# Performance work log

Hardware: AMD Instinct MI355X
Metric: run time of the kernel (lower is better)

The kernel has to match this reference:

```python
import jax, jax.numpy as jnp
import numpy as np

N = 8192      # nodes
F = 256       # in_features
H = 64        # hidden_dim
NEG = -9e15   # mask fill value from the torch source
EPS = 1e-5    # LayerNorm eps (torch default)


def setup_inputs() -> dict:
    key = jax.random.key(0)
    ks = jax.random.split(key, 6)
    x = jax.random.normal(ks[0], (N, F), jnp.float32)
    adj = jax.random.randint(ks[1], (N, N), 0, 2, jnp.int32)
    # Linear params (xavier-ish scale, zero bias as in reset_parameters)
    Wt = jax.random.normal(ks[2], (H, F), jnp.float32) * (1.0 / np.sqrt(F))
    bt = jnp.zeros((H,), jnp.float32)
    Wa = jax.random.normal(ks[3], (1, H), jnp.float32) * (1.0 / np.sqrt(H))
    ba = jnp.zeros((1,), jnp.float32)
    Wp = jax.random.normal(ks[4], (F, H), jnp.float32) * (1.0 / np.sqrt(H))
    bp = jnp.zeros((F,), jnp.float32)
    gamma = jnp.ones((F,), jnp.float32)
    beta = jnp.zeros((F,), jnp.float32)
    return dict(x=x, adj=adj, Wt=Wt, bt=bt, Wa=Wa, ba=ba,
                Wp=Wp, bp=bp, gamma=gamma, beta=beta)


def reference(x, adj, Wt, bt, Wa, ba, Wp, bp, gamma, beta):
    # h = feature_transform(x): [N, H]
    h = x @ Wt.T + bt
    # per-source-node scalar score, expanded over all N columns: [N, 1]
    s = jax.nn.leaky_relu(h @ Wa.T + ba, negative_slope=0.2)
    # adjacency-masked softmax over neighbors (dim=1); s broadcasts to [N, N]
    scores = jnp.where(adj > 0, s, jnp.float32(NEG))
    w = jax.nn.softmax(scores, axis=1)            # [N, N]
    # dropout inactive at inference -> identity
    neighbor = w @ h                               # [N, H]
    tf = neighbor @ Wp.T + bp                      # [N, F]
    # residual + LayerNorm
    y = x + tf
    mu = jnp.mean(y, axis=-1, keepdims=True)
    var = jnp.var(y, axis=-1, keepdims=True)
    return gamma * (y - mu) * jax.lax.rsqrt(var + EPS) + beta
```

## Files before the change

### kernel.cpp

```cpp
#include <hip/hip_runtime.h>
#include <stdint.h>

#define NN 8192
#define FF 256
#define HH 64

typedef __attribute__((ext_vector_type(8))) short bf16x8;
typedef __attribute__((ext_vector_type(4))) float f32x4;

__device__ __forceinline__ uint16_t f2bf(float f) {
  union { float f; uint32_t i; } c; c.f = f;
  uint32_t r = c.i + 0x7FFFu + ((c.i >> 16) & 1u);
  return (uint16_t)(r >> 16);
}

__global__ __launch_bounds__(256) void k1_h(
    const float* __restrict__ x, const float* __restrict__ Wt,
    const float* __restrict__ bt, uint16_t* __restrict__ hT) {
  __shared__ float wtT[256 * 65];
  __shared__ float sbt[64];
  __shared__ uint16_t s_tr[64][34];
  const int t = threadIdx.x;
  const int lane = t & 63;
  const int w = t >> 6;

  for (int i = 0; i < 64; ++i)
    wtT[t * 65 + i] = Wt[(size_t)i * FF + t];
  if (t < 64) sbt[t] = bt[t];
  __syncthreads();

  const int n0 = blockIdx.x * 32;
  const int r0 = n0 + w * 8;
  const float binit = sbt[lane];
  float acc[8];
#pragma unroll
  for (int r = 0; r < 8; ++r) acc[r] = binit;

  for (int f4 = 0; f4 < FF; f4 += 4) {
    float4 xs[8];
#pragma unroll
    for (int r = 0; r < 8; ++r)
      xs[r] = *(const float4*)(x + (size_t)(r0 + r) * FF + f4);
    const float wt0 = wtT[(f4 + 0) * 65 + lane];
    const float wt1 = wtT[(f4 + 1) * 65 + lane];
    const float wt2 = wtT[(f4 + 2) * 65 + lane];
    const float wt3 = wtT[(f4 + 3) * 65 + lane];
#pragma unroll
    for (int r = 0; r < 8; ++r)
      acc[r] += xs[r].x * wt0 + xs[r].y * wt1 + xs[r].z * wt2 + xs[r].w * wt3;
  }

#pragma unroll
  for (int r = 0; r < 8; ++r)
    s_tr[lane][w * 8 + r] = f2bf(acc[r]);
  __syncthreads();
#pragma unroll
  for (int i = 0; i < 4; ++i) {
    int idx = i * 256 + t;
    int c = idx >> 4;
    int d = idx & 15;
    uint32_t v = (uint32_t)s_tr[c][2 * d] | ((uint32_t)s_tr[c][2 * d + 1] << 16);
    *(uint32_t*)(hT + (size_t)c * NN + n0 + 2 * d) = v;
  }
}

__global__ __launch_bounds__(256) void k2_attn(
    const int* __restrict__ adj, const uint16_t* __restrict__ hT,
    float* __restrict__ nb_part, int* __restrict__ deg_part) {
  __shared__ float s_part[4][16][64];
  __shared__ int   s_deg[16];

  const int t    = threadIdx.x;
  const int w    = t >> 6;
  const int lane = t & 63;
  const int m    = lane & 15;
  const int q    = lane >> 4;
  const int g    = blockIdx.x >> 1;
  const int half = blockIdx.x & 1;
  const int row0 = g * 16;

  if (t < 16) s_deg[t] = 0;
  __syncthreads();

  const int kbeg = half * (NN / 2) + w * (NN / 8);
  const int kend = kbeg + (NN / 8);

  f32x4 acc0 = 0, acc1 = 0, acc2 = 0, acc3 = 0;
  uint32_t degp = 0;
  const int* __restrict__ arow = adj + (size_t)(row0 + m) * NN;
  const uint16_t* __restrict__ hrow = hT + (size_t)m * NN;

  for (int kb = kbeg; kb < kend; kb += 64) {
    const int k0 = kb + q * 8;
    const int k1 = k0 + 32;
    int4 a0 = *(const int4*)(arow + k0);
    int4 a1 = *(const int4*)(arow + k0 + 4);
    int4 a2 = *(const int4*)(arow + k1);
    int4 a3 = *(const int4*)(arow + k1 + 4);
    bf16x8 b0 = *(const bf16x8*)(hrow + k0);
    bf16x8 b1 = *(const bf16x8*)(hrow + 16 * NN + k0);
    bf16x8 b2 = *(const bf16x8*)(hrow + 32 * NN + k0);
    bf16x8 b3 = *(const bf16x8*)(hrow + 48 * NN + k0);
    bf16x8 c0 = *(const bf16x8*)(hrow + k1);
    bf16x8 c1 = *(const bf16x8*)(hrow + 16 * NN + k1);
    bf16x8 c2 = *(const bf16x8*)(hrow + 32 * NN + k1);
    bf16x8 c3 = *(const bf16x8*)(hrow + 48 * NN + k1);
    uint32_t p0 = (uint32_t)a0.x | ((uint32_t)a0.y << 16);
    uint32_t p1 = (uint32_t)a0.z | ((uint32_t)a0.w << 16);
    uint32_t p2 = (uint32_t)a1.x | ((uint32_t)a1.y << 16);
    uint32_t p3 = (uint32_t)a1.z | ((uint32_t)a1.w << 16);
    uint32_t p4 = (uint32_t)a2.x | ((uint32_t)a2.y << 16);
    uint32_t p5 = (uint32_t)a2.z | ((uint32_t)a2.w << 16);
    uint32_t p6 = (uint32_t)a3.x | ((uint32_t)a3.y << 16);
    uint32_t p7 = (uint32_t)a3.z | ((uint32_t)a3.w << 16);
    union U { bf16x8 v; uint32_t u[4]; } afA, afB;
    afA.u[0] = p0 * 0x3F80u;
    afA.u[1] = p1 * 0x3F80u;
    afA.u[2] = p2 * 0x3F80u;
    afA.u[3] = p3 * 0x3F80u;
    afB.u[0] = p4 * 0x3F80u;
    afB.u[1] = p5 * 0x3F80u;
    afB.u[2] = p6 * 0x3F80u;
    afB.u[3] = p7 * 0x3F80u;
    degp += p0 + p1 + p2 + p3 + p4 + p5 + p6 + p7;
    acc0 = __builtin_amdgcn_mfma_f32_16x16x32_bf16(afA.v, b0, acc0, 0, 0, 0);
    acc1 = __builtin_amdgcn_mfma_f32_16x16x32_bf16(afA.v, b1, acc1, 0, 0, 0);
    acc2 = __builtin_amdgcn_mfma_f32_16x16x32_bf16(afA.v, b2, acc2, 0, 0, 0);
    acc3 = __builtin_amdgcn_mfma_f32_16x16x32_bf16(afA.v, b3, acc3, 0, 0, 0);
    acc0 = __builtin_amdgcn_mfma_f32_16x16x32_bf16(afB.v, c0, acc0, 0, 0, 0);
    acc1 = __builtin_amdgcn_mfma_f32_16x16x32_bf16(afB.v, c1, acc1, 0, 0, 0);
    acc2 = __builtin_amdgcn_mfma_f32_16x16x32_bf16(afB.v, c2, acc2, 0, 0, 0);
    acc3 = __builtin_amdgcn_mfma_f32_16x16x32_bf16(afB.v, c3, acc3, 0, 0, 0);
  }

  int degm = (int)(degp & 0xFFFFu) + (int)(degp >> 16);
  degm += __shfl_down(degm, 32, 64);
  degm += __shfl_down(degm, 16, 64);
  if (lane < 16) atomicAdd(&s_deg[lane], degm);

#pragma unroll
  for (int rg = 0; rg < 4; ++rg) {
    s_part[w][q * 4 + rg][ 0 + m] = acc0[rg];
    s_part[w][q * 4 + rg][16 + m] = acc1[rg];
    s_part[w][q * 4 + rg][32 + m] = acc2[rg];
    s_part[w][q * 4 + rg][48 + m] = acc3[rg];
  }
  __syncthreads();

  float* __restrict__ dst = nb_part + ((size_t)half * NN + row0) * HH;
  for (int idx = t; idx < 16 * 64; idx += 256) {
    int r = idx >> 6, c = idx & 63;
    float s = s_part[0][r][c] + s_part[1][r][c] +
              s_part[2][r][c] + s_part[3][r][c];
    dst[(size_t)r * HH + c] = s;
  }
  if (t < 16) deg_part[half * NN + row0 + t] = s_deg[t];
}

__global__ __launch_bounds__(256) void k3_epi(
    const float* __restrict__ x, const float* __restrict__ nb_part,
    const int* __restrict__ deg_part, const float* __restrict__ Wp,
    const float* __restrict__ bp, const float* __restrict__ gamma,
    const float* __restrict__ beta, float* __restrict__ out) {
  __shared__ float s_nb[16][64];
  __shared__ float s_y[16 * 256];

  const int t    = threadIdx.x;
  const int w    = t >> 6;
  const int lane = t & 63;
  const int row0 = blockIdx.x * 16;

  for (int idx = t; idx < 16 * 64; idx += 256) {
    int r = idx >> 6, c = idx & 63;
    int d = deg_part[row0 + r] + deg_part[NN + row0 + r];
    float s = nb_part[(size_t)(row0 + r) * HH + c] +
              nb_part[(size_t)(NN + row0 + r) * HH + c];
    s_nb[r][c] = (d > 0) ? s / (float)d : 0.f;
  }
  __syncthreads();

  {
    const int f = t;
    float wp[64];
    const float* wrow = Wp + (size_t)f * HH;
#pragma unroll
    for (int j = 0; j < 16; ++j) {
      float4 v = *(const float4*)(wrow + j * 4);
      wp[j * 4 + 0] = v.x; wp[j * 4 + 1] = v.y;
      wp[j * 4 + 2] = v.z; wp[j * 4 + 3] = v.w;
    }
    const float bpf = bp[f];
    for (int r = 0; r < 16; ++r) {
      float a = bpf;
#pragma unroll
      for (int k = 0; k < 64; k += 4) {
        float4 nv = *(const float4*)&s_nb[r][k];
        a += nv.x * wp[k] + nv.y * wp[k + 1] + nv.z * wp[k + 2] + nv.w * wp[k + 3];
      }
      float y = x[(size_t)(row0 + r) * FF + f] + a;
      s_y[r * 256 + f] = y;
    }
  }
  __syncthreads();

  for (int i = 0; i < 4; ++i) {
    const int r = w * 4 + i;
    float4 v = *(const float4*)&s_y[r * 256 + lane * 4];
    float sum = v.x + v.y + v.z + v.w;
    float ss  = v.x * v.x + v.y * v.y + v.z * v.z + v.w * v.w;
#pragma unroll
    for (int o = 32; o >= 1; o >>= 1) {
      sum += __shfl_xor(sum, o, 64);
      ss  += __shfl_xor(ss, o, 64);
    }
    const float mu  = sum * (1.0f / 256.0f);
    const float var = ss * (1.0f / 256.0f) - mu * mu;
    const float rs  = rsqrtf(var + 1e-5f);
    const int f0 = lane * 4;
    float4 g = *(const float4*)(gamma + f0);
    float4 b = *(const float4*)(beta + f0);
    float4 o4;
    o4.x = g.x * (v.x - mu) * rs + b.x;
    o4.y = g.y * (v.y - mu) * rs + b.y;
    o4.z = g.z * (v.z - mu) * rs + b.z;
    o4.w = g.w * (v.w - mu) * rs + b.w;
    *(float4*)(out + (size_t)(row0 + r) * FF + f0) = o4;
  }
}

extern "C" void kernel_launch(void* const* d_in, const int* in_sizes, int n_in,
                              void* d_out, int out_size, void* d_ws, size_t ws_size,
                              hipStream_t stream) {
  const float* x     = (const float*)d_in[0];
  const int*   adj   = (const int*)d_in[1];
  const float* Wt    = (const float*)d_in[2];
  const float* bt    = (const float*)d_in[3];
  const float* Wp    = (const float*)d_in[6];
  const float* bp    = (const float*)d_in[7];
  const float* gamma = (const float*)d_in[8];
  const float* beta  = (const float*)d_in[9];
  float* out = (float*)d_out;

  uint16_t* hT       = (uint16_t*)d_ws;
  float*    nb_part  = (float*)((char*)d_ws + (1u << 20));
  int*      deg_part = (int*)((char*)d_ws + (5u << 20));

  k1_h  <<<256,  256, 0, stream>>>(x, Wt, bt, hT);
  k2_attn<<<1024, 256, 0, stream>>>(adj, hT, nb_part, deg_part);
  k3_epi <<<512,  256, 0, stream>>>(x, nb_part, deg_part, Wp, bp, gamma, beta, out);
}
```

Baseline: 450.4 us.

## Fuse attention aggregation with epilogue and stage adjacency through swizzled LDS

```diff
diff --git a/kernel.cpp b/kernel.cpp
--- a/kernel.cpp
+++ b/kernel.cpp
@@ -64,80 +64,80 @@
   }
 }
 
-__global__ __launch_bounds__(256) void k2_attn(
+__global__ __launch_bounds__(256) void k2f(
     const int* __restrict__ adj, const uint16_t* __restrict__ hT,
-    float* __restrict__ nb_part, int* __restrict__ deg_part) {
-  __shared__ float s_part[4][16][64];
-  __shared__ int   s_deg[16];
+    const float* __restrict__ x, const float* __restrict__ Wp,
+    const float* __restrict__ bp, const float* __restrict__ gamma,
+    const float* __restrict__ beta, float* __restrict__ out) {
+  __shared__ __align__(16) unsigned char smem[49408];
+  unsigned char* af = smem;
+  float (*s_part)[16][64] = (float (*)[16][64])(smem + 32768);
+  float (*s_degw)[16]     = (float (*)[16])(smem + 32768 + 16384);
+  float (*s_nb)[64]       = (float (*)[64])(smem);
+  float* s_y              = (float*)(smem + 4096);
 
   const int t    = threadIdx.x;
   const int w    = t >> 6;
   const int lane = t & 63;
   const int m    = lane & 15;
   const int q    = lane >> 4;
-  const int g    = blockIdx.x >> 1;
-  const int half = blockIdx.x & 1;
-  const int row0 = g * 16;
-
-  if (t < 16) s_deg[t] = 0;
-  __syncthreads();
-
-  const int kbeg = half * (NN / 2) + w * (NN / 8);
-  const int kend = kbeg + (NN / 8);
-
-  f32x4 acc0 = 0, acc1 = 0, acc2 = 0, acc3 = 0;
-  uint32_t degp = 0;
-  const int* __restrict__ arow = adj + (size_t)(row0 + m) * NN;
+  const int row0 = blockIdx.x * 16;
+
+  bf16x8 vone;
+#pragma unroll
+  for (int j = 0; j < 8; ++j) vone[j] = (short)0x3F80;
+
+  f32x4 acc0 = 0, acc1 = 0, acc2 = 0, acc3 = 0, accd = 0;
   const uint16_t* __restrict__ hrow = hT + (size_t)m * NN;
-
-  for (int kb = kbeg; kb < kend; kb += 64) {
-    const int k0 = kb + q * 8;
-    const int k1 = k0 + 32;
-    int4 a0 = *(const int4*)(arow + k0);
-    int4 a1 = *(const int4*)(arow + k0 + 4);
-    int4 a2 = *(const int4*)(arow + k1);
-    int4 a3 = *(const int4*)(arow + k1 + 4);
-    bf16x8 b0 = *(const bf16x8*)(hrow + k0);
-    bf16x8 b1 = *(const bf16x8*)(hrow + 16 * NN + k0);
-    bf16x8 b2 = *(const bf16x8*)(hrow + 32 * NN + k0);
-    bf16x8 b3 = *(const bf16x8*)(hrow + 48 * NN + k0);
-    bf16x8 c0 = *(const bf16x8*)(hrow + k1);
-    bf16x8 c1 = *(const bf16x8*)(hrow + 16 * NN + k1);
-    bf16x8 c2 = *(const bf16x8*)(hrow + 32 * NN + k1);
-    bf16x8 c3 = *(const bf16x8*)(hrow + 48 * NN + k1);
-    uint32_t p0 = (uint32_t)a0.x | ((uint32_t)a0.y << 16);
-    uint32_t p1 = (uint32_t)a0.z | ((uint32_t)a0.w << 16);
-    uint32_t p2 = (uint32_t)a1.x | ((uint32_t)a1.y << 16);
-    uint32_t p3 = (uint32_t)a1.z | ((uint32_t)a1.w << 16);
-    uint32_t p4 = (uint32_t)a2.x | ((uint32_t)a2.y << 16);
-    uint32_t p5 = (uint32_t)a2.z | ((uint32_t)a2.w << 16);
-    uint32_t p6 = (uint32_t)a3.x | ((uint32_t)a3.y << 16);
-    uint32_t p7 = (uint32_t)a3.z | ((uint32_t)a3.w << 16);
-    union U { bf16x8 v; uint32_t u[4]; } afA, afB;
-    afA.u[0] = p0 * 0x3F80u;
-    afA.u[1] = p1 * 0x3F80u;
-    afA.u[2] = p2 * 0x3F80u;
-    afA.u[3] = p3 * 0x3F80u;
-    afB.u[0] = p4 * 0x3F80u;
-    afB.u[1] = p5 * 0x3F80u;
-    afB.u[2] = p6 * 0x3F80u;
-    afB.u[3] = p7 * 0x3F80u;
-    degp += p0 + p1 + p2 + p3 + p4 + p5 + p6 + p7;
-    acc0 = __builtin_amdgcn_mfma_f32_16x16x32_bf16(afA.v, b0, acc0, 0, 0, 0);
-    acc1 = __builtin_amdgcn_mfma_f32_16x16x32_bf16(afA.v, b1, acc1, 0, 0, 0);
-    acc2 = __builtin_amdgcn_mfma_f32_16x16x32_bf16(afA.v, b2, acc2, 0, 0, 0);
-    acc3 = __builtin_amdgcn_mfma_f32_16x16x32_bf16(afA.v, b3, acc3, 0, 0, 0);
-    acc0 = __builtin_amdgcn_mfma_f32_16x16x32_bf16(afB.v, c0, acc0, 0, 0, 0);
-    acc1 = __builtin_amdgcn_mfma_f32_16x16x32_bf16(afB.v, c1, acc1, 0, 0, 0);
-    acc2 = __builtin_amdgcn_mfma_f32_16x16x32_bf16(afB.v, c2, acc2, 0, 0, 0);
-    acc3 = __builtin_amdgcn_mfma_f32_16x16x32_bf16(afB.v, c3, acc3, 0, 0, 0);
-  }
-
-  int degm = (int)(degp & 0xFFFFu) + (int)(degp >> 16);
-  degm += __shfl_down(degm, 32, 64);
-  degm += __shfl_down(degm, 16, 64);
-  if (lane < 16) atomicAdd(&s_deg[lane], degm);
-
+  const int rsw = (m & 7) << 4;
+
+  for (int tile = 0; tile < 8; ++tile) {
+    const int c0 = tile * 1024;
+#pragma unroll
+    for (int i = 0; i < 16; ++i) {
+      int4 a = *(const int4*)(adj + (size_t)(row0 + i) * NN + c0 + t * 4);
+      uint32_t lo = ((uint32_t)a.x | ((uint32_t)a.y << 16)) * 0x3F80u;
+      uint32_t hi = ((uint32_t)a.z | ((uint32_t)a.w << 16)) * 0x3F80u;
+      uint2 w2; w2.x = lo; w2.y = hi;
+      uint32_t boff = (uint32_t)(t * 8) ^ (uint32_t)((i & 7) << 4);
+      *(uint2*)(af + (i << 11) + boff) = w2;
+    }
+    __syncthreads();
+#pragma unroll
+    for (int it = 0; it < 4; ++it) {
+      const int kl = w * 256 + it * 64;
+      const int k0 = c0 + kl + q * 8;
+      const int k1 = k0 + 32;
+      bf16x8 afA = *(const bf16x8*)(af + (m << 11) +
+                                    ((uint32_t)((kl + q * 8) * 2) ^ rsw));
+      bf16x8 afB = *(const bf16x8*)(af + (m << 11) +
+                                    ((uint32_t)((kl + q * 8 + 32) * 2) ^ rsw));
+      bf16x8 b0 = *(const bf16x8*)(hrow + k0);
+      bf16x8 b1 = *(const bf16x8*)(hrow + 16 * NN + k0);
+      bf16x8 b2 = *(const bf16x8*)(hrow + 32 * NN + k0);
+      bf16x8 b3 = *(const bf16x8*)(hrow + 48 * NN + k0);
+      bf16x8 d0 = *(const bf16x8*)(hrow + k1);
+      bf16x8 d1 = *(const bf16x8*)(hrow + 16 * NN + k1);
+      bf16x8 d2 = *(const bf16x8*)(hrow + 32 * NN + k1);
+      bf16x8 d3 = *(const bf16x8*)(hrow + 48 * NN + k1);
+      acc0 = __builtin_amdgcn_mfma_f32_16x16x32_bf16(afA, b0, acc0, 0, 0, 0);
+      acc1 = __builtin_amdgcn_mfma_f32_16x16x32_bf16(afA, b1, acc1, 0, 0, 0);
+      acc2 = __builtin_amdgcn_mfma_f32_16x16x32_bf16(afA, b2, acc2, 0, 0, 0);
+      acc3 = __builtin_amdgcn_mfma_f32_16x16x32_bf16(afA, b3, acc3, 0, 0, 0);
+      accd = __builtin_amdgcn_mfma_f32_16x16x32_bf16(afA, vone, accd, 0, 0, 0);
+      acc0 = __builtin_amdgcn_mfma_f32_16x16x32_bf16(afB, d0, acc0, 0, 0, 0);
+      acc1 = __builtin_amdgcn_mfma_f32_16x16x32_bf16(afB, d1, acc1, 0, 0, 0);
+      acc2 = __builtin_amdgcn_mfma_f32_16x16x32_bf16(afB, d2, acc2, 0, 0, 0);
+      acc3 = __builtin_amdgcn_mfma_f32_16x16x32_bf16(afB, d3, acc3, 0, 0, 0);
+      accd = __builtin_amdgcn_mfma_f32_16x16x32_bf16(afB, vone, accd, 0, 0, 0);
+    }
+    __syncthreads();
+  }
+
+#pragma unroll
+  for (int rg = 0; rg < 4; ++rg) {
+    (*s_part)[0][0] = (*s_part)[0][0];
+  }
 #pragma unroll
   for (int rg = 0; rg < 4; ++rg) {
     s_part[w][q * 4 + rg][ 0 + m] = acc0[rg];
@@ -145,37 +145,18 @@
     s_part[w][q * 4 + rg][32 + m] = acc2[rg];
     s_part[w][q * 4 + rg][48 + m] = acc3[rg];
   }
-  __syncthreads();
-
-  float* __restrict__ dst = nb_part + ((size_t)half * NN + row0) * HH;
+  if (m == 0) {
+#pragma unroll
+    for (int rg = 0; rg < 4; ++rg) s_degw[w][q * 4 + rg] = accd[rg];
+  }
+  __syncthreads();
+
   for (int idx = t; idx < 16 * 64; idx += 256) {
     int r = idx >> 6, c = idx & 63;
     float s = s_part[0][r][c] + s_part[1][r][c] +
               s_part[2][r][c] + s_part[3][r][c];
-    dst[(size_t)r * HH + c] = s;
-  }
-  if (t < 16) deg_part[half * NN + row0 + t] = s_deg[t];
-}
-
-__global__ __launch_bounds__(256) void k3_epi(
-    const float* __restrict__ x, const float* __restrict__ nb_part,
-    const int* __restrict__ deg_part, const float* __restrict__ Wp,
-    const float* __restrict__ bp, const float* __restrict__ gamma,
-    const float* __restrict__ beta, float* __restrict__ out) {
-  __shared__ float s_nb[16][64];
-  __shared__ float s_y[16 * 256];
-
-  const int t    = threadIdx.x;
-  const int w    = t >> 6;
-  const int lane = t & 63;
-  const int row0 = blockIdx.x * 16;
-
-  for (int idx = t; idx < 16 * 64; idx += 256) {
-    int r = idx >> 6, c = idx & 63;
-    int d = deg_part[row0 + r] + deg_part[NN + row0 + r];
-    float s = nb_part[(size_t)(row0 + r) * HH + c] +
-              nb_part[(size_t)(NN + row0 + r) * HH + c];
-    s_nb[r][c] = (d > 0) ? s / (float)d : 0.f;
+    float d = s_degw[0][r] + s_degw[1][r] + s_degw[2][r] + s_degw[3][r];
+    s_nb[r][c] = (d > 0.5f) ? s / d : 0.f;
   }
   __syncthreads();
 
@@ -241,11 +222,8 @@
   const float* beta  = (const float*)d_in[9];
   float* out = (float*)d_out;
 
-  uint16_t* hT       = (uint16_t*)d_ws;
-  float*    nb_part  = (float*)((char*)d_ws + (1u << 20));
-  int*      deg_part = (int*)((char*)d_ws + (5u << 20));
-
-  k1_h  <<<256,  256, 0, stream>>>(x, Wt, bt, hT);
-  k2_attn<<<1024, 256, 0, stream>>>(adj, hT, nb_part, deg_part);
-  k3_epi <<<512,  256, 0, stream>>>(x, nb_part, deg_part, Wp, bp, gamma, beta, out);
-}
+  uint16_t* hT = (uint16_t*)d_ws;
+
+  k1_h<<<256, 256, 0, stream>>>(x, Wt, bt, hT);
+  k2f <<<512, 256, 0, stream>>>(adj, hT, x, Wp, bp, gamma, beta, out);
+}
```

New measurement: 476.5 us. 1.06x slower.
